# Optimization experiments

Hardware: AMD Instinct MI355X
Metric: run time of the kernel (lower is better)

Reference implementation:

```python
import jax, jax.numpy as jnp
import numpy as np

B, N, D_IN, D_OUT, H = 2, 2048, 1024, 1024, 16
HEAD_DIM = D_OUT // H


def setup_inputs() -> dict:
    key = jax.random.key(0)
    ks = jax.random.split(key, 8)
    s = 0.02
    return {
        "x": jax.random.normal(ks[0], (B, N, D_IN), dtype=jnp.float32),
        "Wq": jax.random.normal(ks[1], (D_IN, D_OUT), dtype=jnp.float32) * s,
        "Wk": jax.random.normal(ks[2], (D_IN, D_OUT), dtype=jnp.float32) * s,
        "Wv": jax.random.normal(ks[3], (D_IN, D_OUT), dtype=jnp.float32) * s,
        "Wo": jax.random.normal(ks[4], (D_OUT, D_OUT), dtype=jnp.float32) * s,
        "bo": jnp.zeros((D_OUT,), dtype=jnp.float32),
        "w": jax.random.uniform(ks[5], (H,), dtype=jnp.float32),
        "v": jax.random.uniform(ks[6], (H,), dtype=jnp.float32),
    }


def reference(x, Wq, Wk, Wv, Wo, bo, w, v):
    b, n, _ = x.shape
    h = w.shape[0]
    hd = Wq.shape[1] // h

    # QKV projections -> [b, h, n, hd]
    def proj(W):
        return (x @ W).reshape(b, n, h, hd).transpose(0, 2, 1, 3)

    q, k, val = proj(Wq), proj(Wk), proj(Wv)

    # relative-distance decay R_hat: [h, n, n]
    pos = jnp.arange(n)
    R = jnp.abs(pos[:, None] - pos[None, :]).astype(x.dtype)  # [n, n]
    wv = w[:, None, None]
    vv = v[:, None, None]
    R_hat = (1.0 + jnp.exp(vv)) / (1.0 + jnp.exp(vv - wv * R))  # [h, n, n]

    # ReLU(QK^T) * R_hat, causal mask, scaled softmax
    scores = jax.nn.relu(jnp.einsum("bhqd,bhkd->bhqk", q, k)) * R_hat[None]
    causal = jnp.triu(jnp.ones((n, n), dtype=bool), k=1)
    scores = jnp.where(causal[None, None], -jnp.inf, scores)
    attn = jax.nn.softmax(scores / np.sqrt(hd).astype(x.dtype), axis=-1)

    ctx = jnp.einsum("bhqk,bhkd->bhqd", attn, val)
    ctx = ctx.transpose(0, 2, 1, 3).reshape(b, n, h * hd)
    return ctx @ Wo + bo
```

## Files before the change

### kernel.cpp

```cpp
#include <hip/hip_runtime.h>

typedef unsigned short u16;
typedef unsigned int u32;
typedef __attribute__((ext_vector_type(8))) short bf16x8;
typedef __attribute__((ext_vector_type(4))) float f32x4;

__device__ __forceinline__ u16 f2bf(float f) {
    u32 u = __float_as_uint(f);
    u += 0x7fffu + ((u >> 16) & 1u);
    return (u16)(u >> 16);
}

__device__ __forceinline__ u32 cvtpk(float lo, float hi) {
    u32 r;
    asm("v_cvt_pk_bf16_f32 %0, %1, %2" : "=v"(r) : "v"(lo), "v"(hi));
    return r;
}

#define GL2LDS(gp, lp)                                                                 \
    __builtin_amdgcn_global_load_lds((const __attribute__((address_space(1))) u32*)(const void*)(gp), \
                                     (__attribute__((address_space(3))) u32*)(void*)(lp), 16, 0, 0)

#define SBAR                                                                           \
    do {                                                                               \
        __builtin_amdgcn_sched_barrier(0);                                             \
        __builtin_amdgcn_s_barrier();                                                  \
        __builtin_amdgcn_sched_barrier(0);                                             \
    } while (0)
#define WAITV(N)                                                                       \
    do {                                                                               \
        asm volatile("s_waitcnt vmcnt(" #N ")" ::: "memory");                          \
        __builtin_amdgcn_sched_barrier(0);                                             \
    } while (0)
#define WAITLGKM0                                                                      \
    do {                                                                               \
        asm volatile("s_waitcnt lgkmcnt(0)" ::: "memory");                             \
        __builtin_amdgcn_sched_barrier(0);                                             \
    } while (0)

__global__ __launch_bounds__(256) void prep_kernel(const float* __restrict__ x,
                                                   const float* __restrict__ Wq,
                                                   const float* __restrict__ Wk,
                                                   const float* __restrict__ Wv,
                                                   const float* __restrict__ Wo,
                                                   const float* __restrict__ wp,
                                                   const float* __restrict__ vp,
                                                   u16* __restrict__ xb,
                                                   u16* __restrict__ Wcat,
                                                   u16* __restrict__ Wot,
                                                   float* __restrict__ tab,
                                                   u32* __restrict__ counter) {
    __shared__ float tl[32][33];
    const int bid = blockIdx.x, t = threadIdx.x;
    if (bid < 4096) {
        const int i = bid * 256 + t;
        float4 val = ((const float4*)x)[i];
        uint2 o;
        o.x = cvtpk(val.x, val.y);
        o.y = cvtpk(val.z, val.w);
        ((uint2*)xb)[i] = o;
    } else if (bid < 8192) {
        const int tid = bid - 4096;
        const int zi = tid >> 10, rem = tid & 1023;
        const int kt = (rem >> 5) * 32, nt = (rem & 31) * 32;
        const float* src = (zi == 0) ? Wq : (zi == 1) ? Wk : (zi == 2) ? Wv : Wo;
        u16* dst = (zi < 3) ? (Wcat + zi * 1048576) : Wot;
        const int tx = t & 31, ty = t >> 5;
#pragma unroll
        for (int j = 0; j < 4; ++j)
            tl[ty + j * 8][tx] = src[(kt + ty + j * 8) * 1024 + nt + tx];
        __syncthreads();
#pragma unroll
        for (int j = 0; j < 4; ++j)
            dst[(nt + ty + j * 8) * 1024 + kt + tx] = f2bf(tl[tx][ty + j * 8]);
    } else {
        const int i = (bid - 8192) * 256 + t;
        if (i == 0) counter[0] = 0u;
        const int h = i >> 11, d = i & 2047;
        const float vv = vp[h], ww = wp[h];
        tab[i] = (1.f + expf(vv)) / (1.f + expf(vv - ww * (float)d)) *
                 (0.125f * 1.44269504088896340736f);
    }
}

__global__ __launch_bounds__(512, 2) void gemm256(const u16* __restrict__ A,
                                                  const u16* __restrict__ Bt,
                                                  u16* __restrict__ Cb,
                                                  u16* __restrict__ Vt) {
    extern __shared__ u16 sm[];
    const int t = threadIdx.x, lane = t & 63, w = t >> 6;
    const int l15 = lane & 15, quad = lane >> 4;
    const int wr = w >> 2, wc = w & 3;
    const int m0 = blockIdx.y << 8, n0 = blockIdx.x << 8;
    const int srow = lane >> 2, sc = lane & 3;

    f32x4 acc[8][4];
#pragma unroll
    for (int i = 0; i < 8; ++i)
#pragma unroll
        for (int j = 0; j < 4; ++j) acc[i][j] = (f32x4){0.f, 0.f, 0.f, 0.f};

    auto stage = [&](int O, int kt, int kh) {
        const u16* src = O ? Bt : A;
        const int g0 = O ? n0 : m0;
        const int base = O * 32768 + (kt & 1) * 16384 + kh * 8192;
        const int k0 = (kt << 6) + (kh << 5);
#pragma unroll
        for (int j = 0; j < 2; ++j) {
            const int row = (w * 2 + j) * 16 + srow;
            const int g = (sc ^ (row & 3)) << 3;
            GL2LDS(src + (size_t)(g0 + row) * 1024 + k0 + g,
                   &sm[base + (w * 2 + j) * 512]);
        }
    };

    auto phase = [&](int d, int mh, int kh, auto&& stg, int wmode) {
        bf16x8 af[4], bf[4];
        const int ab = d * 16384 + kh * 8192;
        const int bb = 32768 + d * 16384 + kh * 8192;
#pragma unroll
        for (int mm = 0; mm < 4; ++mm) {
            const int row = wr * 128 + mh * 64 + mm * 16 + l15;
            af[mm] = *(const bf16x8*)&sm[ab + row * 32 + ((quad ^ (row & 3)) << 3)];
        }
#pragma unroll
        for (int nn = 0; nn < 4; ++nn) {
            const int row = wc * 64 + nn * 16 + l15;
            bf[nn] = *(const bf16x8*)&sm[bb + row * 32 + ((quad ^ (row & 3)) << 3)];
        }
        stg();
        SBAR;
        WAITLGKM0;
        __builtin_amdgcn_s_setprio(1);
#pragma unroll
        for (int mm = 0; mm < 4; ++mm)
#pragma unroll
            for (int nn = 0; nn < 4; ++nn)
                acc[mh * 4 + mm][nn] = __builtin_amdgcn_mfma_f32_16x16x32_bf16(
                    af[mm], bf[nn], acc[mh * 4 + mm][nn], 0, 0, 0);
        __builtin_amdgcn_s_setprio(0);
        if (wmode == 1) WAITV(8);
        else if (wmode == 2) WAITV(4);
        else if (wmode == 3) WAITV(0);
        SBAR;
    };

    stage(0, 0, 0); stage(1, 0, 0); stage(0, 0, 1); stage(1, 0, 1);
    stage(0, 1, 0); stage(1, 1, 0);
    WAITV(8);
    SBAR;

    for (int i = 0; i < 8; ++i) {
        const bool nl = (i < 7);
        phase(0, 0, 0, [&] { stage(0, 2 * i + 1, 1); }, 0);
        phase(0, 1, 0, [&] { stage(1, 2 * i + 1, 1); }, 1);
        phase(0, 0, 1, [&] { if (nl) stage(0, 2 * i + 2, 0); }, 0);
        phase(0, 1, 1, [&] { if (nl) stage(1, 2 * i + 2, 0); }, nl ? 1 : 2);
        phase(1, 0, 0, [&] { if (nl) stage(0, 2 * i + 2, 1); }, 0);
        phase(1, 1, 0, [&] { if (nl) stage(1, 2 * i + 2, 1); }, nl ? 1 : 3);
        phase(1, 0, 1, [&] { if (nl) stage(0, 2 * i + 3, 0); }, 0);
        phase(1, 1, 1, [&] { if (nl) stage(1, 2 * i + 3, 0); }, nl ? 1 : 0);
    }

    const int cb0 = n0 + wc * 64;
#pragma unroll
    for (int am = 0; am < 8; ++am) {
#pragma unroll
        for (int nn = 0; nn < 4; ++nn) {
            const int col = cb0 + nn * 16 + l15;
            if (n0 < 2048) {
                const int row = m0 + wr * 128 + am * 16 + (quad << 2);
#pragma unroll
                for (int r = 0; r < 4; ++r)
                    Cb[(size_t)(row + r) * 2048 + col] = f2bf(acc[am][nn][r]);
            } else {
                const int mm = am & 3, mh = am >> 2;
                const int win = m0 + wr * 128 + mh * 64;
                const int pos = (((mm >> 1) * 4 + quad) << 3) + ((mm & 1) << 2);
                uint2 o;
                o.x = cvtpk(acc[am][nn][0], acc[am][nn][1]);
                o.y = cvtpk(acc[am][nn][2], acc[am][nn][3]);
                *(uint2*)(Vt + (size_t)(col - 2048) * 4096 + win + pos) = o;
            }
        }
    }
}

template <int MODE, int BN>
__global__ __launch_bounds__(256, 3) void gemm128(const u16* __restrict__ A,
                                                  const u16* __restrict__ Bt,
                                                  float* __restrict__ C,
                                                  const float* __restrict__ bias,
                                                  int M, int N, int K) {
    constexpr int NBW = BN / 32;
    __shared__ __align__(16) u16 As[8192];
    __shared__ __align__(16) u16 Bs[BN * 64];
    const int t = threadIdx.x, lane = t & 63, wv = t >> 6;
    const int l15 = lane & 15, quad = lane >> 4;
    const int m0 = blockIdx.y << 7, n0 = blockIdx.x * BN;
    const int wm = (wv & 1) << 6, wn = (wv >> 1) * (BN / 2);

    f32x4 acc[4][NBW];
#pragma unroll
    for (int i = 0; i < 4; ++i)
#pragma unroll
        for (int j = 0; j < NBW; ++j) acc[i][j] = (f32x4){0.f, 0.f, 0.f, 0.f};

    const int lrow = lane >> 3, lchunk = lane & 7;
    for (int k0 = 0; k0 < K; k0 += 64) {
#pragma unroll
        for (int c = 0; c < 4; ++c) {
            const int r0 = wv * 32 + c * 8;
            const int row = r0 + lrow;
            const int g = lchunk ^ (row & 7);
            GL2LDS(A + (size_t)(m0 + row) * K + k0 + g * 8, &As[r0 * 64]);
        }
#pragma unroll
        for (int c = 0; c < BN / 32; ++c) {
            const int r0 = wv * (BN / 4) + c * 8;
            const int row = r0 + lrow;
            const int g = lchunk ^ (row & 7);
            GL2LDS(Bt + (size_t)(n0 + row) * K + k0 + g * 8, &Bs[r0 * 64]);
        }
        __syncthreads();
#pragma unroll
        for (int ks = 0; ks < 2; ++ks) {
            const int p = ((ks << 2) | quad) ^ (l15 & 7);
            bf16x8 af[4], bfr[NBW];
#pragma unroll
            for (int i = 0; i < 4; ++i)
                af[i] = *(const bf16x8*)&As[(wm + i * 16 + l15) * 64 + p * 8];
#pragma unroll
            for (int j = 0; j < NBW; ++j)
                bfr[j] = *(const bf16x8*)&Bs[(wn + j * 16 + l15) * 64 + p * 8];
#pragma unroll
            for (int mb = 0; mb < 4; ++mb)
#pragma unroll
                for (int nb = 0; nb < NBW; ++nb)
                    acc[mb][nb] = __builtin_amdgcn_mfma_f32_16x16x32_bf16(af[mb], bfr[nb],
                                                                          acc[mb][nb], 0, 0, 0);
        }
        __syncthreads();
    }
    const int rb = m0 + wm + (quad << 2);
    const int cbase = n0 + wn + l15;
#pragma unroll
    for (int mb = 0; mb < 4; ++mb)
#pragma unroll
        for (int nb = 0; nb < NBW; ++nb) {
            const int col = cbase + nb * 16;
#pragma unroll
            for (int r = 0; r < 4; ++r) {
                const int row = rb + mb * 16 + r;
                C[(size_t)row * N + col] = acc[mb][nb][r] + bias[col];
            }
        }
}

__global__ __launch_bounds__(256, 3) void attn_kernel(const u16* __restrict__ qkb,
                                                      const u16* __restrict__ vtb,
                                                      const float* __restrict__ rtab,
                                                      u16* __restrict__ ctxb,
                                                      u32* __restrict__ counter) {
    __shared__ __align__(16) u16 Kt[3][4096];
    __shared__ __align__(16) u16 Vt2[2][4096];
    __shared__ __align__(16) float rall[2048];
    __shared__ int jobS;

    const int t = threadIdx.x, lane = t & 63, wv = t >> 6;
    const int l15 = lane & 15, quad = lane >> 4;
    const int lrow = lane >> 3, lchunk = lane & 7;
    const int half0 = (wv & 1) * 32;

    for (;;) {
        if (t == 0) jobS = (int)atomicAdd(counter, 1u);
        __syncthreads();
        const int job = jobS;
        if (job >= 1024) break;
        const int qt = 31 - (job >> 5);
        const int bh = job & 31;
        const int b = bh >> 4, h = bh & 15;
        const int q0 = qt << 6;

        {
            const float4* src = (const float4*)(rtab + (h << 11));
            const int nf = (q0 + 64) >> 2;
            for (int i = t; i < nf; i += 256) ((float4*)rall)[i] = src[i];
        }

        bf16x8 qb[2];
        {
            const u16* qrow = qkb + (size_t)(b * 2048 + q0 + (wv << 4) + l15) * 2048 +
                              (h << 6) + quad * 8;
            qb[0] = *(const bf16x8*)(qrow);
            qb[1] = *(const bf16x8*)(qrow + 32);
        }

        auto stage_k = [&](int ktile, int kb) {
#pragma unroll
            for (int c = 0; c < 4; ++c) {
                const int r0 = half0 + c * 8;
                const int row = r0 + lrow;
                const int g = lchunk ^ (row & 7);
                GL2LDS(qkb + (size_t)(b * 2048 + (ktile << 6) + row) * 2048 + 1024 +
                           (h << 6) + g * 8,
                       &Kt[kb][r0 * 64]);
            }
        };
        auto stage_v = [&](int ktile, int vb) {
#pragma unroll
            for (int c = 0; c < 4; ++c) {
                const int r0 = half0 + c * 8;
                const int row = r0 + lrow;
                const int g = lchunk ^ (row & 7);
                GL2LDS(vtb + (size_t)((h << 6) + row) * 4096 + b * 2048 + (ktile << 6) +
                           g * 8,
                       &Vt2[vb][r0 * 64]);
            }
        };

        f32x4 cacc[4];
#pragma unroll
        for (int i = 0; i < 4; ++i) cacc[i] = (f32x4){0.f, 0.f, 0.f, 0.f};
        f32x4 lacc4 = (f32x4){0.f, 0.f, 0.f, 0.f};

        if (wv < 2) {
            stage_k(0, 0);
            if (qt >= 1) stage_k(1, 1);
        } else {
            stage_v(0, 0);
        }
        WAITLGKM0;

        for (int kt = 0; kt <= qt; ++kt) {
            const int kb = kt % 3, vb = kt & 1;
            if (wv < 2) {
                if (kt < qt) WAITV(4);
                else         WAITV(0);
            }
            SBAR;
            if (wv < 2) {
                if (kt + 2 <= qt) stage_k(kt + 2, (kt + 2) % 3);
            } else {
                if (kt + 1 <= qt) stage_v(kt + 1, (kt + 1) & 1);
            }

            f32x4 sacc[4];
#pragma unroll
            for (int i = 0; i < 4; ++i) sacc[i] = (f32x4){0.f, 0.f, 0.f, 0.f};
            __builtin_amdgcn_s_setprio(1);
#pragma unroll
            for (int ks = 0; ks < 2; ++ks) {
                const int p = ((ks << 2) | quad) ^ (l15 & 7);
#pragma unroll
                for (int mb = 0; mb < 4; ++mb) {
                    bf16x8 ka = *(const bf16x8*)&Kt[kb][(mb * 16 + l15) * 64 + p * 8];
                    sacc[mb] = __builtin_amdgcn_mfma_f32_16x16x32_bf16(ka, qb[ks],
                                                                       sacc[mb], 0, 0, 0);
                }
            }
            __builtin_amdgcn_s_setprio(0);

            const int D0 = q0 - (kt << 6) + (wv << 4) + l15;
            u32 pk[4][2];
            if (kt < qt) {
#pragma unroll
                for (int mb = 0; mb < 4; ++mb) {
                    float pe[4];
#pragma unroll
                    for (int r = 0; r < 4; ++r) {
                        const int dist = D0 - (mb * 16 + (quad << 2) + r);
                        pe[r] = exp2f(fmaxf(sacc[mb][r], 0.f) * rall[dist]);
                        lacc4[r] += pe[r];
                    }
                    pk[mb][0] = cvtpk(pe[0], pe[1]);
                    pk[mb][1] = cvtpk(pe[2], pe[3]);
                }
            } else {
#pragma unroll
                for (int mb = 0; mb < 4; ++mb) {
                    float pe[4];
#pragma unroll
                    for (int r = 0; r < 4; ++r) {
                        const int dist = D0 - (mb * 16 + (quad << 2) + r);
                        const int di = dist < 0 ? 0 : dist;
                        float p0 = exp2f(fmaxf(sacc[mb][r], 0.f) * rall[di]);
                        pe[r] = (dist < 0) ? 0.f : p0;
                        lacc4[r] += pe[r];
                    }
                    pk[mb][0] = cvtpk(pe[0], pe[1]);
                    pk[mb][1] = cvtpk(pe[2], pe[3]);
                }
            }

            if (wv >= 2) {
                if (kt < qt) WAITV(4);
                else         WAITV(0);
            }
            SBAR;

            __builtin_amdgcn_s_setprio(1);
#pragma unroll
            for (int ks = 0; ks < 2; ++ks) {
                int4 pv = {(int)pk[2 * ks][0], (int)pk[2 * ks][1],
                           (int)pk[2 * ks + 1][0], (int)pk[2 * ks + 1][1]};
                bf16x8 pb = *(bf16x8*)&pv;
                const int g = (4 * ks + quad) ^ (l15 & 7);
#pragma unroll
                for (int db = 0; db < 4; ++db) {
                    bf16x8 vf = *(const bf16x8*)&Vt2[vb][(db * 16 + l15) * 64 + g * 8];
                    cacc[db] = __builtin_amdgcn_mfma_f32_16x16x32_bf16(vf, pb,
                                                                       cacc[db], 0, 0, 0);
                }
            }
            __builtin_amdgcn_s_setprio(0);
        }

        float lt = (lacc4[0] + lacc4[1]) + (lacc4[2] + lacc4[3]);
        lt += __shfl_xor(lt, 16, 64);
        lt += __shfl_xor(lt, 32, 64);
        const float inv = 1.f / lt;
        u16* op = ctxb + (size_t)(b * 2048 + q0 + (wv << 4) + l15) * 1024 +
                  (h << 6) + (quad << 2);
#pragma unroll
        for (int db = 0; db < 4; ++db) {
            uint2 o;
            o.x = cvtpk(cacc[db][0] * inv, cacc[db][1] * inv);
            o.y = cvtpk(cacc[db][2] * inv, cacc[db][3] * inv);
            *(uint2*)(op + db * 16) = o;
        }
    }
}

extern "C" void kernel_launch(void* const* d_in, const int* in_sizes, int n_in,
                              void* d_out, int out_size, void* d_ws, size_t ws_size,
                              hipStream_t stream) {
    const float* x  = (const float*)d_in[0];
    const float* Wq = (const float*)d_in[1];
    const float* Wk = (const float*)d_in[2];
    const float* Wv = (const float*)d_in[3];
    const float* Wo = (const float*)d_in[4];
    const float* bo = (const float*)d_in[5];
    const float* w  = (const float*)d_in[6];
    const float* v  = (const float*)d_in[7];
    float* out = (float*)d_out;

    char* w8 = (char*)d_ws;
    u16*  xb   = (u16*)(w8);
    u16*  Wcat = (u16*)(w8 + (8u << 20));
    u16*  Wot  = (u16*)(w8 + (14u << 20));
    u16*  qkb  = (u16*)(w8 + (16u << 20));
    u16*  vtb  = (u16*)(w8 + (32u << 20));
    u16*  ctxb = (u16*)(w8 + (40u << 20));
    float* rtab = (float*)(w8 + (48u << 20));
    u32*  counter = (u32*)(w8 + (48u << 20) + (1u << 17));

    static bool attrSet = false;
    if (!attrSet) {
        hipFuncSetAttribute(reinterpret_cast<const void*>(gemm256),
                            hipFuncAttributeMaxDynamicSharedMemorySize, 131072);
        attrSet = true;
    }

    prep_kernel<<<8320, 256, 0, stream>>>(x, Wq, Wk, Wv, Wo, w, v, xb, Wcat, Wot, rtab,
                                          counter);
    gemm256<<<dim3(12, 16), 512, 131072, stream>>>(xb, Wcat, qkb, vtb);
    attn_kernel<<<768, 256, 0, stream>>>(qkb, vtb, rtab, ctxb, counter);
    gemm128<0, 64><<<dim3(16, 32), 256, 0, stream>>>(ctxb, Wot, out, bo, 4096, 1024, 1024);
}
```

Measured before the change: 196.3 us.

## Restructure QKV GEMM LDS staging into full-k-tile units with XCD-aware block remap

The 256x256 GEMM now stages whole 64-wide k tiles as four 128-row units with an 8-chunk XOR swizzle, replacing the previous fine-grained half-k staging interleaved across eight phases. All loads for the next tile are issued in the first phase of each k step, and only the last phase waits for them. Block indices are also remapped so that consecutive blocks on the same XCD share rows and columns for L2 reuse. In exchange the prefetch is coarser, and the global loads may be exposed more at the single full wait per tile.

```diff
diff --git a/kernel.cpp b/kernel.cpp
--- a/kernel.cpp
+++ b/kernel.cpp
@@ -91,8 +91,11 @@
     const int t = threadIdx.x, lane = t & 63, w = t >> 6;
     const int l15 = lane & 15, quad = lane >> 4;
     const int wr = w >> 2, wc = w & 3;
-    const int m0 = blockIdx.y << 8, n0 = blockIdx.x << 8;
-    const int srow = lane >> 2, sc = lane & 3;
+    const int bid0 = blockIdx.y * 12 + blockIdx.x;
+    const int bid = (bid0 & 7) * 24 + (bid0 >> 3);
+    const int bx = bid % 12, by = bid / 12;
+    const int m0 = by << 8, n0 = bx << 8;
+    const int srow8 = lane >> 3, schunk = lane & 7;
 
     f32x4 acc[8][4];
 #pragma unroll
@@ -100,35 +103,41 @@
 #pragma unroll
         for (int j = 0; j < 4; ++j) acc[i][j] = (f32x4){0.f, 0.f, 0.f, 0.f};
 
-    auto stage = [&](int O, int kt, int kh) {
+    auto stageu = [&](int O, int d, int hh, int kt) {
         const u16* src = O ? Bt : A;
-        const int g0 = O ? n0 : m0;
-        const int base = O * 32768 + (kt & 1) * 16384 + kh * 8192;
-        const int k0 = (kt << 6) + (kh << 5);
+        const int g0 = (O ? n0 : m0) + hh * 128;
+        u16* base = &sm[(O * 4 + d * 2 + hh) * 8192];
+        const int k0 = kt << 6;
 #pragma unroll
         for (int j = 0; j < 2; ++j) {
-            const int row = (w * 2 + j) * 16 + srow;
-            const int g = (sc ^ (row & 3)) << 3;
-            GL2LDS(src + (size_t)(g0 + row) * 1024 + k0 + g,
-                   &sm[base + (w * 2 + j) * 512]);
+            const int rl = (w * 2 + j) * 8 + srow8;
+            const int g = schunk ^ (rl & 7);
+            GL2LDS(src + (size_t)(g0 + rl) * 1024 + k0 + g * 8,
+                   base + (w * 2 + j) * 512);
         }
     };
-
-    auto phase = [&](int d, int mh, int kh, auto&& stg, int wmode) {
+    auto stage_tile = [&](int kt) {
+        const int d = kt & 1;
+        stageu(0, d, 0, kt); stageu(0, d, 1, kt);
+        stageu(1, d, 0, kt); stageu(1, d, 1, kt);
+    };
+
+    auto phase = [&](int d, int mh, int ks, bool dostage, int kstage, bool dowait) {
+        const u16* Au = &sm[(d * 2 + wr) * 8192];
+        const u16* Bu = &sm[(4 + d * 2 + (wc >> 1)) * 8192];
+        const int p = (ks << 2) | quad;
         bf16x8 af[4], bf[4];
-        const int ab = d * 16384 + kh * 8192;
-        const int bb = 32768 + d * 16384 + kh * 8192;
 #pragma unroll
         for (int mm = 0; mm < 4; ++mm) {
-            const int row = wr * 128 + mh * 64 + mm * 16 + l15;
-            af[mm] = *(const bf16x8*)&sm[ab + row * 32 + ((quad ^ (row & 3)) << 3)];
+            const int rl = mh * 64 + mm * 16 + l15;
+            af[mm] = *(const bf16x8*)&Au[rl * 64 + ((p ^ (l15 & 7)) << 3)];
         }
 #pragma unroll
         for (int nn = 0; nn < 4; ++nn) {
-            const int row = wc * 64 + nn * 16 + l15;
-            bf[nn] = *(const bf16x8*)&sm[bb + row * 32 + ((quad ^ (row & 3)) << 3)];
-        }
-        stg();
+            const int rl = (wc & 1) * 64 + nn * 16 + l15;
+            bf[nn] = *(const bf16x8*)&Bu[rl * 64 + ((p ^ (l15 & 7)) << 3)];
+        }
+        if (dostage) stage_tile(kstage);
         SBAR;
         WAITLGKM0;
         __builtin_amdgcn_s_setprio(1);
@@ -139,27 +148,21 @@
                 acc[mh * 4 + mm][nn] = __builtin_amdgcn_mfma_f32_16x16x32_bf16(
                     af[mm], bf[nn], acc[mh * 4 + mm][nn], 0, 0, 0);
         __builtin_amdgcn_s_setprio(0);
-        if (wmode == 1) WAITV(8);
-        else if (wmode == 2) WAITV(4);
-        else if (wmode == 3) WAITV(0);
+        if (dowait) WAITV(0);
         SBAR;
     };
 
-    stage(0, 0, 0); stage(1, 0, 0); stage(0, 0, 1); stage(1, 0, 1);
-    stage(0, 1, 0); stage(1, 1, 0);
-    WAITV(8);
+    stage_tile(0);
+    WAITV(0);
     SBAR;
 
-    for (int i = 0; i < 8; ++i) {
-        const bool nl = (i < 7);
-        phase(0, 0, 0, [&] { stage(0, 2 * i + 1, 1); }, 0);
-        phase(0, 1, 0, [&] { stage(1, 2 * i + 1, 1); }, 1);
-        phase(0, 0, 1, [&] { if (nl) stage(0, 2 * i + 2, 0); }, 0);
-        phase(0, 1, 1, [&] { if (nl) stage(1, 2 * i + 2, 0); }, nl ? 1 : 2);
-        phase(1, 0, 0, [&] { if (nl) stage(0, 2 * i + 2, 1); }, 0);
-        phase(1, 1, 0, [&] { if (nl) stage(1, 2 * i + 2, 1); }, nl ? 1 : 3);
-        phase(1, 0, 1, [&] { if (nl) stage(0, 2 * i + 3, 0); }, 0);
-        phase(1, 1, 1, [&] { if (nl) stage(1, 2 * i + 3, 0); }, nl ? 1 : 0);
+    for (int kt = 0; kt < 16; ++kt) {
+        const int d = kt & 1;
+        const bool nl = (kt < 15);
+        phase(d, 0, 0, nl, kt + 1, false);
+        phase(d, 0, 1, false, 0, false);
+        phase(d, 1, 0, false, 0, false);
+        phase(d, 1, 1, false, 0, nl);
     }
 
     const int cb0 = n0 + wc * 64;
```

After: 194.7 us. No clear change (-0.8%).
